# Performance work log

Measured on AMD Instinct MI355X. Metric: run time of the kernel, lower is better.

Reference implementation:

```python
import jax, jax.numpy as jnp
import numpy as np

WS = 7           # window_size
DIM_HEAD = 32    # qk head dim
NUM_HEAD = 8     # dim_in // dim_head = 256 // 32
DIM_EXP = 1024   # dim_in * exp_ratio
WIN_NUM = 16     # (28 // 7) ** 2
EPS = 1e-5


def _rel_pos_index():
    # same construction as torch buffer; returns [49*49] int index into (2*WS-1)^2 table
    coords = np.stack(np.meshgrid(np.arange(WS), np.arange(WS), indexing='ij'))  # [2,WS,WS]
    cf = coords.reshape(2, -1)                                                   # [2,49]
    rel = cf[:, :, None] - cf[:, None, :]                                        # [2,49,49]
    rel = rel.transpose(1, 2, 0)
    rel[:, :, 0] += WS - 1
    rel[:, :, 1] += WS - 1
    rel[:, :, 0] *= 2 * WS - 1
    return jnp.asarray(rel.sum(-1).reshape(-1), dtype=jnp.int32)                 # [2401]


def _ln_channel(x, w, b):
    # LayerNorm over channel dim (axis=1) of [b,c,h,w], per the 'ln_1d' norm
    mu = jnp.mean(x, axis=1, keepdims=True)
    var = jnp.var(x, axis=1, keepdims=True)
    xn = (x - mu) * jax.lax.rsqrt(var + EPS)
    return xn * w[None, :, None, None] + b[None, :, None, None]


def setup_inputs() -> dict:
    key = jax.random.key(0)
    ks = jax.random.split(key, 12)
    C = 256
    x = jax.random.normal(ks[0], (64, C, 28, 28), dtype=jnp.float32)
    return {
        'x': x,
        'pre_w': jnp.ones((C,), jnp.float32),
        'pre_b': jnp.zeros((C,), jnp.float32),
        'qk_w': jax.random.normal(ks[1], (2 * C, C), jnp.float32) * 0.02,
        'qk_b': jnp.zeros((2 * C,), jnp.float32),
        'v_w': jax.random.normal(ks[2], (DIM_EXP, C), jnp.float32) * 0.02,
        'v_b': jnp.zeros((DIM_EXP,), jnp.float32),
        'post_w': jnp.ones((DIM_EXP // 2,), jnp.float32),
        'post_b': jnp.zeros((DIM_EXP // 2,), jnp.float32),
        'proj_w': jax.random.normal(ks[3], (C, DIM_EXP), jnp.float32) * 0.02,
        'proj_b': jnp.zeros((C,), jnp.float32),
        'rpb_table': jax.random.normal(ks[4], (WIN_NUM, (2 * WS - 1) ** 2, NUM_HEAD), jnp.float32) * 0.02,
    }


def reference(x, pre_w, pre_b, qk_w, qk_b, v_w, v_b, post_w, post_b, proj_w, proj_b, rpb_table):
    B, C, H, W = x.shape
    n1, n2 = H // WS, W // WS
    shortcut = x
    # b c (h1 n1) (w1 n2) -> (b n1 n2) c h1 w1
    xw = x.reshape(B, C, WS, n1, WS, n2).transpose(0, 3, 5, 1, 2, 4).reshape(B * n1 * n2, C, WS, WS)
    b = B * n1 * n2
    xw = _ln_channel(xw, pre_w, pre_b)
    # 1x1 conv QK -> split into q,k per head: channels ordered (qk, heads, dim_head)
    qk = jnp.einsum('oc,bchw->bohw', qk_w, xw) + qk_b[None, :, None, None]
    qk = qk.reshape(b, 2, NUM_HEAD, DIM_HEAD, WS * WS).transpose(1, 0, 2, 4, 3)  # [2,b,h,49,dh]
    q, k = qk[0], qk[1]
    # 1x1 conv V -> attn half + idle half
    v = jnp.einsum('oc,bchw->bohw', v_w, xw) + v_b[None, :, None, None]
    v_attn, v_idle = jnp.split(v, 2, axis=1)                                     # each [b,512,7,7]
    dhv = (DIM_EXP // 2) // NUM_HEAD
    va = v_attn.reshape(b, NUM_HEAD, dhv, WS * WS).transpose(0, 1, 3, 2)         # [b,h,49,dhv]
    # relative position bias (gathered fresh each forward, one table per window)
    idx = _rel_pos_index()
    bias = rpb_table[:, idx, :]                                                  # [wn,2401,nh]
    bias = bias.reshape(WIN_NUM, WS * WS, WS * WS, NUM_HEAD).transpose(0, 3, 1, 2)
    bias = jnp.broadcast_to(bias[None], (B, WIN_NUM, NUM_HEAD, WS * WS, WS * WS)).reshape(b, NUM_HEAD, WS * WS, WS * WS)
    # SDPA (scale = 1/sqrt(q head dim), additive float mask)
    scale = DIM_HEAD ** -0.5
    logits = jnp.einsum('bhqd,bhkd->bhqk', q, k) * scale + bias
    attn = jax.nn.softmax(logits, axis=-1)
    out = jnp.einsum('bhqk,bhkd->bhqd', attn, va)                                # [b,h,49,dhv]
    out = out.transpose(0, 1, 3, 2).reshape(b, DIM_EXP // 2, WS, WS)
    out = _ln_channel(out, post_w, post_b)
    xc = jnp.concatenate([out, v_idle], axis=1)                                  # [b,dim_exp,7,7]
    # (b n1 n2) c h1 w1 -> b c (h1 n1) (w1 n2)
    xc = xc.reshape(B, n1, n2, DIM_EXP, WS, WS).transpose(0, 3, 4, 1, 5, 2).reshape(B, DIM_EXP, H, W)
    xc = jax.nn.gelu(xc, approximate=False)
    xc = jnp.einsum('oc,bchw->bohw', proj_w, xc) + proj_b[None, :, None, None]
    y = shortcut + xc
    return jnp.roll(y, shift=(2, 2), axis=(2, 3))
```

## Files before the change

kernel.cpp:

```cpp
#include <hip/hip_runtime.h>
#include <hip/hip_bf16.h>

typedef __bf16          bf16x8 __attribute__((ext_vector_type(8)));
typedef float           f32x4  __attribute__((ext_vector_type(4)));
typedef unsigned int    u32x2  __attribute__((ext_vector_type(2)));
typedef unsigned int    u32x4v __attribute__((ext_vector_type(4)));

#define QKW_OFF  0
#define VW_OFF   262144
#define PJW_OFF  786432
#define BIAS_OFF 1310720
#define TEMP_OFF 3407872
#define XT_OFF   70516736

#define MFMA(a,b,c) __builtin_amdgcn_mfma_f32_16x16x32_bf16((a),(b),(c),0,0,0)
#define ZERO4 ((f32x4){0.f,0.f,0.f,0.f})
#define CBAR() asm volatile("" ::: "memory")

#define SXN_AT(row, byte)      ((((row)*512 + (byte))) ^ ((((row)&7))<<4))
#define RGB(j)                 (25088 + (j)*6400)
#define RG_AT(base, row, byte) (((base) + (row)*128 + (byte)) ^ (((row)&7)<<4))
#define SC_AT(row, byte)       ((25088 + (row)*512 + (byte)) ^ (((row)&7)<<4))
#define TP_AT(row, byte)       ((((row)*256 + (byte))) ^ (((row)&15)<<4))

static __device__ __forceinline__ unsigned cvtpk(float lo, float hi){
  unsigned r;
  asm("v_cvt_pk_bf16_f32 %0, %1, %2" : "=v"(r) : "v"(lo), "v"(hi));
  return r;
}
static __device__ __forceinline__ unsigned short f2bu(float f) {
  unsigned u = __builtin_bit_cast(unsigned, f);
  return (unsigned short)((u + 0x7FFFu + ((u >> 16) & 1u)) >> 16);
}
static __device__ __forceinline__ float gelu_f(float v){
  return v / (1.f + __expf(-1.5957691216057308f*v*(1.f + 0.044715f*v*v)));
}

__global__ void emo_prep_w(const float* __restrict__ qk_w, const float* __restrict__ v_w,
                           const float* __restrict__ proj_w, unsigned short* __restrict__ w16) {
  int i = blockIdx.x * 256 + threadIdx.x;
  if (i >= 655360) return;
  float v;
  if (i < 131072)      v = qk_w[i];
  else if (i < 393216) v = v_w[i - 131072];
  else                 v = proj_w[i - 393216];
  unsigned u = __builtin_bit_cast(unsigned, v);
  w16[i] = (unsigned short)((u + 0x7FFFu + ((u >> 16) & 1u)) >> 16);
}

__global__ void emo_prep_bias(const float* __restrict__ rpb, float* __restrict__ bx) {
  const int wh = blockIdx.x;
  const int win = wh >> 3, h = wh & 7;
  for (int e = threadIdx.x; e < 4096; e += 256) {
    const int chunk = e >> 8, lane = (e >> 2) & 63, r = e & 3;
    const int mt = chunk >> 2, nt = chunk & 3;
    const int m = mt*16 + (lane >> 4)*4 + r;
    const int n = nt*16 + (lane & 15);
    float v;
    if (n >= 49)      v = -1e30f;
    else if (m >= 49) v = 0.f;
    else {
      const int dI = m/7 - n/7 + 6;
      const int dJ = m%7 - n%7 + 6;
      v = rpb[(win*169 + dI*13 + dJ)*8 + h];
    }
    bx[wh*4096 + e] = v;
  }
}

__global__ __launch_bounds__(256)
void emo_prep_x(const float* __restrict__ x, const float* __restrict__ pre_w,
                const float* __restrict__ pre_b, unsigned short* __restrict__ xt) {
  __shared__ float lv[32*257];
  __shared__ float ps1[8][32];
  __shared__ float ps2[8][32];
  const int tid = threadIdx.x, lane = tid & 63, wv = tid >> 6;
  const int l32 = lane & 31, hp = lane >> 5;
  const int chunk = blockIdx.x, b = blockIdx.y;
  const int s = chunk*32 + l32;
  const bool ok = s < 784;
  const float* xb = x + (size_t)b*200704;
  float s1 = 0.f, s2 = 0.f;
  const int c0 = wv*64 + hp*32;
  for (int ci = 0; ci < 32; ++ci) {
    const int c = c0 + ci;
    const float v = ok ? xb[c*784 + s] : 0.f;
    lv[l32*257 + c] = v;
    s1 += v; s2 += v*v;
  }
  ps1[wv*2 + hp][l32] = s1;
  ps2[wv*2 + hp][l32] = s2;
  __syncthreads();
  const int px = tid & 31, j = tid >> 5;
  const int sp = chunk*32 + px;
  if (sp < 784) {
    float t1 = 0.f, t2 = 0.f;
    #pragma unroll
    for (int k = 0; k < 8; ++k) { t1 += ps1[k][px]; t2 += ps2[k][px]; }
    const float mu = t1*(1.f/256.f);
    const float rs = rsqrtf(t2*(1.f/256.f) - mu*mu + 1e-5f);
    const int h = sp/28, w = sp - h*28;
    const int win = (h & 3)*4 + (w & 3);
    const int wpx = (h >> 2)*7 + (w >> 2);
    unsigned short* row = xt + (((size_t)b*16 + win)*49 + wpx)*256 + j*32;
    #pragma unroll
    for (int g = 0; g < 4; ++g) {
      float gg[8];
      #pragma unroll
      for (int i2 = 0; i2 < 8; ++i2) {
        const int c = j*32 + g*8 + i2;
        gg[i2] = (lv[px*257 + c] - mu)*rs*pre_w[c] + pre_b[c];
      }
      u32x4v pk = { cvtpk(gg[0],gg[1]), cvtpk(gg[2],gg[3]), cvtpk(gg[4],gg[5]), cvtpk(gg[6],gg[7]) };
      *(u32x4v*)(row + g*8) = pk;
    }
  }
}

__global__ __launch_bounds__(512, 4)
void emo_main(const float* __restrict__ qk_b,  const float* __restrict__ v_b,
              const float* __restrict__ post_w,const float* __restrict__ post_b,
              const char*  __restrict__ wsc,
              float* __restrict__ temp)
{
  extern __shared__ char smem[];
  const int tid  = threadIdx.x;
  const int lane = tid & 63;
  const int l16  = lane & 15;
  const int lk   = lane >> 4;
  const int wv   = tid >> 6;
  const int bid  = blockIdx.x;
  const int Bi   = (bid >> 3) & 63;
  const int win  = ((bid & 7) << 1) | (bid >> 9);
  const int SCR  = RGB(wv);

  {
    const unsigned short* xw = (const unsigned short*)(wsc + XT_OFF)
                             + ((size_t)Bi*16 + win)*(49*256);
    for (int p = wv; p < 49; p += 8) {
      const u32x2 d = *(const u32x2*)(xw + p*256 + lane*4);
      *(u32x2*)(smem + SXN_AT(p, lane*8)) = d;
    }
  }
  __syncthreads();

  f32x4 aq[2][4], ak[2][4];
  #pragma unroll
  for (int mt = 0; mt < 2; ++mt)
    #pragma unroll
    for (int nt = 0; nt < 4; ++nt) { aq[mt][nt] = ZERO4; ak[mt][nt] = ZERO4; }
  #pragma unroll 2
  for (int kt = 0; kt < 8; ++kt) {
    bf16x8 bx[4];
    #pragma unroll
    for (int nt = 0; nt < 4; ++nt) {
      const int row = nt*16 + l16, rc = row < 49 ? row : 48;
      bx[nt] = *(const bf16x8*)(smem + SXN_AT(rc, kt*64 + lk*16));
    }
    #pragma unroll
    for (int mt = 0; mt < 2; ++mt) {
      const bf16x8 awq = *(const bf16x8*)(wsc + QKW_OFF + (size_t)(      wv*32 + mt*16 + l16)*512 + kt*64 + lk*16);
      const bf16x8 awk = *(const bf16x8*)(wsc + QKW_OFF + (size_t)(256 + wv*32 + mt*16 + l16)*512 + kt*64 + lk*16);
      #pragma unroll
      for (int nt = 0; nt < 4; ++nt) {
        aq[mt][nt] = MFMA(awq, bx[nt], aq[mt][nt]);
        ak[mt][nt] = MFMA(awk, bx[nt], ak[mt][nt]);
      }
    }
  }
  {
    const f32x4 bq0 = *(const f32x4*)(qk_b +       wv*32 +      lk*4);
    const f32x4 bq1 = *(const f32x4*)(qk_b +       wv*32 + 16 + lk*4);
    const f32x4 bk0 = *(const f32x4*)(qk_b + 256 + wv*32 +      lk*4);
    const f32x4 bk1 = *(const f32x4*)(qk_b + 256 + wv*32 + 16 + lk*4);
    #pragma unroll
    for (int nt = 0; nt < 4; ++nt) {
      aq[0][nt] += bq0; aq[1][nt] += bq1; ak[0][nt] += bk0; ak[1][nt] += bk1;
    }
  }

  #pragma unroll
  for (int nt = 0; nt < 4; ++nt) {
    const int px = nt*16 + l16;
    if (px < 49) {
      #pragma unroll
      for (int mt = 0; mt < 2; ++mt) {
        u32x2 pq  = { cvtpk(aq[mt][nt][0], aq[mt][nt][1]), cvtpk(aq[mt][nt][2], aq[mt][nt][3]) };
        u32x2 pk2 = { cvtpk(ak[mt][nt][0], ak[mt][nt][1]), cvtpk(ak[mt][nt][2], ak[mt][nt][3]) };
        *(u32x2*)(smem + RG_AT(SCR, px,      (mt*16 + lk*4)*2)) = pq;
        *(u32x2*)(smem + RG_AT(SCR, px, 64 + (mt*16 + lk*4)*2)) = pk2;
      }
    }
  }
  CBAR();

  bf16x8 qa[4], kb[4];
  #pragma unroll
  for (int t = 0; t < 4; ++t) {
    const int row = t*16 + l16, rc = row < 49 ? row : 48;
    qa[t] = *(const bf16x8*)(smem + RG_AT(SCR, rc,      lk*16));
    kb[t] = *(const bf16x8*)(smem + RG_AT(SCR, rc, 64 + lk*16));
  }

  f32x4 s[4][4];
  {
    const float scale = 0.17677669529663689f;
    const float* bxp = (const float*)(wsc + BIAS_OFF) + (size_t)(win*8 + wv)*4096 + lane*4;
    #pragma unroll
    for (int mt = 0; mt < 4; ++mt)
      #pragma unroll
      for (int nt = 0; nt < 4; ++nt) {
        f32x4 z = MFMA(qa[mt], kb[nt], ZERO4);
        s[mt][nt] = z*scale + *(const f32x4*)(bxp + (mt*4 + nt)*256);
      }
  }
  #pragma unroll
  for (int mt = 0; mt < 4; ++mt) {
    #pragma unroll
    for (int r = 0; r < 4; ++r) {
      float mx = fmaxf(fmaxf(s[mt][0][r], s[mt][1][r]), fmaxf(s[mt][2][r], s[mt][3][r]));
      mx = fmaxf(mx, __shfl_xor(mx, 1)); mx = fmaxf(mx, __shfl_xor(mx, 2));
      mx = fmaxf(mx, __shfl_xor(mx, 4)); mx = fmaxf(mx, __shfl_xor(mx, 8));
      const float e0 = __expf(s[mt][0][r]-mx), e1 = __expf(s[mt][1][r]-mx);
      const float e2 = __expf(s[mt][2][r]-mx), e3 = __expf(s[mt][3][r]-mx);
      float sm = e0+e1+e2+e3;
      sm += __shfl_xor(sm, 1); sm += __shfl_xor(sm, 2);
      sm += __shfl_xor(sm, 4); sm += __shfl_xor(sm, 8);
      const float inv = 1.f/sm;
      s[mt][0][r] = e0*inv; s[mt][1][r] = e1*inv;
      s[mt][2][r] = e2*inv; s[mt][3][r] = e3*inv;
    }
  }
  #pragma unroll
  for (int mt = 0; mt < 4; ++mt)
    #pragma unroll
    for (int r = 0; r < 4; ++r) {
      const int q = mt*16 + lk*4 + r;
      if (q < 49) {
        #pragma unroll
        for (int nt = 0; nt < 4; ++nt)
          *(unsigned short*)(smem + RG_AT(SCR, q, (nt*16 + l16)*2)) = f2bu(s[mt][nt][r]);
      }
    }
  CBAR();

  f32x4 av[4][4];
  #pragma unroll
  for (int mt = 0; mt < 4; ++mt)
    #pragma unroll
    for (int nt = 0; nt < 4; ++nt) av[mt][nt] = ZERO4;
  #pragma unroll 2
  for (int kt = 0; kt < 8; ++kt) {
    bf16x8 ax[4], bw[4];
    #pragma unroll
    for (int t = 0; t < 4; ++t) {
      const int row = t*16 + l16, rc = row < 49 ? row : 48;
      ax[t] = *(const bf16x8*)(smem + SXN_AT(rc, kt*64 + lk*16));
      bw[t] = *(const bf16x8*)(wsc + VW_OFF + (size_t)(wv*64 + t*16 + l16)*512 + kt*64 + lk*16);
    }
    #pragma unroll
    for (int mt = 0; mt < 4; ++mt)
      #pragma unroll
      for (int nt = 0; nt < 4; ++nt) av[mt][nt] = MFMA(ax[mt], bw[nt], av[mt][nt]);
  }
  {
    #pragma unroll
    for (int nt = 0; nt < 4; ++nt) {
      const float vb = v_b[wv*64 + nt*16 + l16];
      #pragma unroll
      for (int mt = 0; mt < 4; ++mt)
        #pragma unroll
        for (int r = 0; r < 4; ++r) av[mt][nt][r] += vb;
    }
  }

  bf16x8 fpb[4][2];
  #pragma unroll
  for (int t = 0; t < 4; ++t) {
    const int row = t*16 + l16, rc = row < 49 ? row : 48;
    #pragma unroll
    for (int kt = 0; kt < 2; ++kt)
      fpb[t][kt] = *(const bf16x8*)(smem + RG_AT(SCR, rc, (kt*32 + lk*8)*2));
  }
  CBAR();

  f32x4 o[4][4];
  #pragma unroll
  for (int h2 = 0; h2 < 2; ++h2) {
    #pragma unroll
    for (int tc = 0; tc < 2; ++tc) {
      const int nt = h2*2 + tc;
      const int chrow = tc*16 + l16;
      #pragma unroll
      for (int mt = 0; mt < 4; ++mt) {
        u32x2 pv = { cvtpk(av[mt][nt][0], av[mt][nt][1]), cvtpk(av[mt][nt][2], av[mt][nt][3]) };
        *(u32x2*)(smem + RG_AT(SCR, chrow, (mt*16 + lk*4)*2)) = pv;
      }
    }
    CBAR();
    #pragma unroll
    for (int tc = 0; tc < 2; ++tc) {
      const int mtc = h2*2 + tc;
      const bf16x8 a0 = *(const bf16x8*)(smem + RG_AT(SCR, tc*16 + l16, (     lk*8)*2));
      const bf16x8 a1 = *(const bf16x8*)(smem + RG_AT(SCR, tc*16 + l16, (32 + lk*8)*2));
      #pragma unroll
      for (int nt = 0; nt < 4; ++nt) {
        f32x4 z = MFMA(a0, fpb[nt][0], ZERO4);
        o[mtc][nt] = MFMA(a1, fpb[nt][1], z);
      }
    }
    CBAR();
  }

  #pragma unroll
  for (int mtc = 0; mtc < 4; ++mtc)
    #pragma unroll
    for (int nt = 0; nt < 4; ++nt) {
      const int q = nt*16 + l16;
      if (q < 49) {
        u32x2 pk = { cvtpk(o[mtc][nt][0], o[mtc][nt][1]), cvtpk(o[mtc][nt][2], o[mtc][nt][3]) };
        *(u32x2*)(smem + RG_AT(RGB(wv), q, (mtc*16 + lk*4)*2)) = pk;
      }
    }
  __syncthreads();

  {
    const int px = tid >> 3, j = tid & 7;
    if (px < 49) {
      bf16x8 f[8];
      float s1 = 0.f, s2 = 0.f;
      #pragma unroll
      for (int c8 = 0; c8 < 8; ++c8) {
        f[c8] = *(const bf16x8*)(smem + RG_AT(RGB(j), px, c8*16));
        #pragma unroll
        for (int i = 0; i < 8; ++i) { const float v = (float)f[c8][i]; s1 += v; s2 += v*v; }
      }
      s1 += __shfl_xor(s1, 1); s1 += __shfl_xor(s1, 2); s1 += __shfl_xor(s1, 4);
      s2 += __shfl_xor(s2, 1); s2 += __shfl_xor(s2, 2); s2 += __shfl_xor(s2, 4);
      const float mu = s1*(1.f/512.f);
      const float rs = rsqrtf(s2*(1.f/512.f) - mu*mu + 1e-5f);
      #pragma unroll
      for (int c8 = 0; c8 < 8; ++c8) {
        const f32x4 pw0 = *(const f32x4*)(post_w + j*64 + c8*8);
        const f32x4 pw1 = *(const f32x4*)(post_w + j*64 + c8*8 + 4);
        const f32x4 pb0 = *(const f32x4*)(post_b + j*64 + c8*8);
        const f32x4 pb1 = *(const f32x4*)(post_b + j*64 + c8*8 + 4);
        float g[8];
        #pragma unroll
        for (int i = 0; i < 8; ++i) {
          const float v = (float)f[c8][i];
          const float w = i < 4 ? pw0[i] : pw1[i-4];
          const float b = i < 4 ? pb0[i] : pb1[i-4];
          g[i] = gelu_f((v-mu)*rs*w + b);
        }
        u32x4v pk = { cvtpk(g[0],g[1]), cvtpk(g[2],g[3]), cvtpk(g[4],g[5]), cvtpk(g[6],g[7]) };
        *(u32x4v*)(smem + RG_AT(RGB(j), px, c8*16)) = pk;
      }
    }
  }
  __syncthreads();

  f32x4 pacc[2][4];
  #pragma unroll
  for (int mt = 0; mt < 2; ++mt)
    #pragma unroll
    for (int nt = 0; nt < 4; ++nt) pacc[mt][nt] = ZERO4;
  for (int j8 = 0; j8 < 8; ++j8) {
    #pragma unroll
    for (int kt2 = 0; kt2 < 2; ++kt2) {
      bf16x8 b[4];
      #pragma unroll
      for (int nt = 0; nt < 4; ++nt) {
        const int row = nt*16 + l16, rc = row < 49 ? row : 48;
        b[nt] = *(const bf16x8*)(smem + RG_AT(RGB(j8), rc, (kt2*32 + lk*8)*2));
      }
      const int kg = j8*64 + kt2*32 + lk*8;
      #pragma unroll
      for (int mt = 0; mt < 2; ++mt) {
        const bf16x8 aw = *(const bf16x8*)(wsc + PJW_OFF + (size_t)(wv*32 + mt*16 + l16)*2048 + kg*2);
        #pragma unroll
        for (int nt = 0; nt < 4; ++nt) pacc[mt][nt] = MFMA(aw, b[nt], pacc[mt][nt]);
      }
    }
  }
  for (int half = 0; half < 2; ++half) {
    __syncthreads();
    f32x4 ia[2][4];
    #pragma unroll
    for (int mt = 0; mt < 2; ++mt)
      #pragma unroll
      for (int nt = 0; nt < 4; ++nt) ia[mt][nt] = ZERO4;
    const int r0 = 512 + half*256 + wv*32;
    #pragma unroll 2
    for (int kt = 0; kt < 8; ++kt) {
      bf16x8 b[4];
      #pragma unroll
      for (int nt = 0; nt < 4; ++nt) {
        const int row = nt*16 + l16, rc = row < 49 ? row : 48;
        b[nt] = *(const bf16x8*)(smem + SXN_AT(rc, kt*64 + lk*16));
      }
      #pragma unroll
      for (int mt = 0; mt < 2; ++mt) {
        const bf16x8 aw = *(const bf16x8*)(wsc + VW_OFF + (size_t)(r0 + mt*16 + l16)*512 + kt*64 + lk*16);
        #pragma unroll
        for (int nt = 0; nt < 4; ++nt) ia[mt][nt] = MFMA(aw, b[nt], ia[mt][nt]);
      }
    }
    #pragma unroll
    for (int mt = 0; mt < 2; ++mt) {
      const f32x4 vb = *(const f32x4*)(v_b + r0 + mt*16 + lk*4);
      #pragma unroll
      for (int nt = 0; nt < 4; ++nt) {
        const int px = nt*16 + l16;
        const int chl = wv*32 + mt*16 + lk*4;
        u32x2 pk = { cvtpk(gelu_f(ia[mt][nt][0]+vb[0]), gelu_f(ia[mt][nt][1]+vb[1])),
                     cvtpk(gelu_f(ia[mt][nt][2]+vb[2]), gelu_f(ia[mt][nt][3]+vb[3])) };
        *(u32x2*)(smem + SC_AT(px, chl*2)) = pk;
      }
    }
    __syncthreads();
    #pragma unroll 2
    for (int kt = 0; kt < 8; ++kt) {
      bf16x8 b[4];
      #pragma unroll
      for (int nt = 0; nt < 4; ++nt) {
        const int row = nt*16 + l16;
        b[nt] = *(const bf16x8*)(smem + SC_AT(row, (kt*32 + lk*8)*2));
      }
      const int kg = 512 + half*256 + kt*32 + lk*8;
      #pragma unroll
      for (int mt = 0; mt < 2; ++mt) {
        const bf16x8 aw = *(const bf16x8*)(wsc + PJW_OFF + (size_t)(wv*32 + mt*16 + l16)*2048 + kg*2);
        #pragma unroll
        for (int nt = 0; nt < 4; ++nt) pacc[mt][nt] = MFMA(aw, b[nt], pacc[mt][nt]);
      }
    }
  }

  __syncthreads();
  {
    #pragma unroll
    for (int mt = 0; mt < 2; ++mt)
      #pragma unroll
      for (int r = 0; r < 4; ++r) {
        const int row = wv*32 + mt*16 + lk*4 + r;
        #pragma unroll
        for (int nt = 0; nt < 4; ++nt)
          *(float*)(smem + TP_AT(row, (nt*16 + l16)*4)) = pacc[mt][nt][r];
      }
    CBAR();
    float* tb = temp + ((size_t)Bi*16 + win)*(256*64);
    #pragma unroll
    for (int rep = 0; rep < 8; ++rep) {
      const int idx = rep*64 + lane;
      const int row = wv*32 + (idx >> 4);
      const int ch  = idx & 15;
      *(f32x4*)(tb + row*64 + ch*4) = *(const f32x4*)(smem + TP_AT(row, ch*16));
    }
  }
}

__global__ __launch_bounds__(512)
void emo_epi(const float* __restrict__ x, const float* __restrict__ temp,
             const float* __restrict__ proj_b, float* __restrict__ out) {
  extern __shared__ float lv[];
  const int b  = blockIdx.x >> 4;
  const int ct = blockIdx.x & 15;
  const int tid = threadIdx.x, lane = tid & 63, wv = tid >> 6;
  const float* tbb = temp + (size_t)b*262144;
  for (int rr = wv; rr < 256; rr += 8) {
    const int win = rr >> 4, cc = rr & 15;
    const float v = tbb[(size_t)(win*256 + ct*16 + cc)*64 + lane];
    if (lane < 49) {
      const int ph = lane / 7, pw = lane - ph*7;
      const int h = ph*4 + (win >> 2), w = pw*4 + (win & 3);
      lv[cc*812 + h*29 + w] = v;
    }
  }
  __syncthreads();
  const float* xb = x + (size_t)b*200704;
  float* ob       = out + (size_t)b*200704;
  for (int cc = 0; cc < 16; ++cc) {
    const int c = ct*16 + cc;
    const float pb = proj_b[c];
    for (int i = tid; i < 784; i += 512) {
      const int h = i / 28, w = i - h*28;
      int hs = h - 2; if (hs < 0) hs += 28;
      int ws2 = w - 2; if (ws2 < 0) ws2 += 28;
      ob[c*784 + i] = xb[c*784 + hs*28 + ws2] + lv[cc*812 + hs*29 + ws2] + pb;
    }
  }
}

extern "C" void kernel_launch(void* const* d_in, const int* in_sizes, int n_in,
                              void* d_out, int out_size, void* d_ws, size_t ws_size,
                              hipStream_t stream) {
  const float* x      = (const float*)d_in[0];
  const float* pre_w  = (const float*)d_in[1];
  const float* pre_b  = (const float*)d_in[2];
  const float* qk_w   = (const float*)d_in[3];
  const float* qk_b   = (const float*)d_in[4];
  const float* v_w    = (const float*)d_in[5];
  const float* v_b    = (const float*)d_in[6];
  const float* post_w = (const float*)d_in[7];
  const float* post_b = (const float*)d_in[8];
  const float* proj_w = (const float*)d_in[9];
  const float* proj_b = (const float*)d_in[10];
  const float* rpb    = (const float*)d_in[11];
  float* outp = (float*)d_out;
  char* wsc = (char*)d_ws;

  hipFuncSetAttribute((const void*)emo_main, hipFuncAttributeMaxDynamicSharedMemorySize, 81920);
  hipFuncSetAttribute((const void*)emo_epi,  hipFuncAttributeMaxDynamicSharedMemorySize, 53248);

  emo_prep_w<<<2560, 256, 0, stream>>>(qk_w, v_w, proj_w, (unsigned short*)wsc);
  emo_prep_bias<<<128, 256, 0, stream>>>(rpb, (float*)(wsc + BIAS_OFF));
  emo_prep_x<<<dim3(25, 64), 256, 0, stream>>>(x, pre_w, pre_b,
                                               (unsigned short*)(wsc + XT_OFF));
  emo_main<<<1024, 512, 76288, stream>>>(qk_b, v_b, post_w, post_b,
                                         (const char*)wsc, (float*)(wsc + TEMP_OFF));
  emo_epi<<<1024, 512, 51968, stream>>>(x, (const float*)(wsc + TEMP_OFF), proj_b, outp);
}
```

Before: 325.7 us.

## Fuse epilogue residual/roll into main kernel and merge weight/bias prep kernels

The main kernel now writes the projection output directly to the final rolled positions, adding the shortcut x and proj bias in registers. This removes the temp buffer round trip and the separate epilogue kernel. The two prep kernels for weights and bias are merged into one launch to cut launch overhead. The cost is scattered, poorly coalesced 4-byte global stores and x loads from the main kernel instead of the epilogue's coalesced row writes.

```diff
diff --git a/kernel.cpp b/kernel.cpp
--- a/kernel.cpp
+++ b/kernel.cpp
@@ -10,7 +10,6 @@
 #define VW_OFF   262144
 #define PJW_OFF  786432
 #define BIAS_OFF 1310720
-#define TEMP_OFF 3407872
 #define XT_OFF   70516736
 
 #define MFMA(a,b,c) __builtin_amdgcn_mfma_f32_16x16x32_bf16((a),(b),(c),0,0,0)
@@ -21,7 +20,6 @@
 #define RGB(j)                 (25088 + (j)*6400)
 #define RG_AT(base, row, byte) (((base) + (row)*128 + (byte)) ^ (((row)&7)<<4))
 #define SC_AT(row, byte)       ((25088 + (row)*512 + (byte)) ^ (((row)&7)<<4))
-#define TP_AT(row, byte)       ((((row)*256 + (byte))) ^ (((row)&15)<<4))
 
 static __device__ __forceinline__ unsigned cvtpk(float lo, float hi){
   unsigned r;
@@ -36,35 +34,37 @@
   return v / (1.f + __expf(-1.5957691216057308f*v*(1.f + 0.044715f*v*v)));
 }
 
-__global__ void emo_prep_w(const float* __restrict__ qk_w, const float* __restrict__ v_w,
-                           const float* __restrict__ proj_w, unsigned short* __restrict__ w16) {
-  int i = blockIdx.x * 256 + threadIdx.x;
-  if (i >= 655360) return;
-  float v;
-  if (i < 131072)      v = qk_w[i];
-  else if (i < 393216) v = v_w[i - 131072];
-  else                 v = proj_w[i - 393216];
-  unsigned u = __builtin_bit_cast(unsigned, v);
-  w16[i] = (unsigned short)((u + 0x7FFFu + ((u >> 16) & 1u)) >> 16);
-}
-
-__global__ void emo_prep_bias(const float* __restrict__ rpb, float* __restrict__ bx) {
-  const int wh = blockIdx.x;
-  const int win = wh >> 3, h = wh & 7;
-  for (int e = threadIdx.x; e < 4096; e += 256) {
-    const int chunk = e >> 8, lane = (e >> 2) & 63, r = e & 3;
-    const int mt = chunk >> 2, nt = chunk & 3;
-    const int m = mt*16 + (lane >> 4)*4 + r;
-    const int n = nt*16 + (lane & 15);
+__global__ void emo_prep_wb(const float* __restrict__ qk_w, const float* __restrict__ v_w,
+                            const float* __restrict__ proj_w, const float* __restrict__ rpb,
+                            unsigned short* __restrict__ w16, float* __restrict__ bx) {
+  const int blk = blockIdx.x;
+  if (blk < 2560) {
+    int i = blk * 256 + threadIdx.x;
+    if (i >= 655360) return;
     float v;
-    if (n >= 49)      v = -1e30f;
-    else if (m >= 49) v = 0.f;
-    else {
-      const int dI = m/7 - n/7 + 6;
-      const int dJ = m%7 - n%7 + 6;
-      v = rpb[(win*169 + dI*13 + dJ)*8 + h];
-    }
-    bx[wh*4096 + e] = v;
+    if (i < 131072)      v = qk_w[i];
+    else if (i < 393216) v = v_w[i - 131072];
+    else                 v = proj_w[i - 393216];
+    unsigned u = __builtin_bit_cast(unsigned, v);
+    w16[i] = (unsigned short)((u + 0x7FFFu + ((u >> 16) & 1u)) >> 16);
+  } else {
+    const int wh = blk - 2560;
+    const int win = wh >> 3, h = wh & 7;
+    for (int e = threadIdx.x; e < 4096; e += 256) {
+      const int chunk = e >> 8, lane = (e >> 2) & 63, r = e & 3;
+      const int mt = chunk >> 2, nt = chunk & 3;
+      const int m = mt*16 + (lane >> 4)*4 + r;
+      const int n = nt*16 + (lane & 15);
+      float v;
+      if (n >= 49)      v = -1e30f;
+      else if (m >= 49) v = 0.f;
+      else {
+        const int dI = m/7 - n/7 + 6;
+        const int dJ = m%7 - n%7 + 6;
+        v = rpb[(win*169 + dI*13 + dJ)*8 + h];
+      }
+      bx[wh*4096 + e] = v;
+    }
   }
 }
 
@@ -118,10 +118,12 @@
 }
 
 __global__ __launch_bounds__(512, 4)
-void emo_main(const float* __restrict__ qk_b,  const float* __restrict__ v_b,
+void emo_main(const float* __restrict__ x,
+              const float* __restrict__ qk_b,  const float* __restrict__ v_b,
               const float* __restrict__ post_w,const float* __restrict__ post_b,
+              const float* __restrict__ proj_b,
               const char*  __restrict__ wsc,
-              float* __restrict__ temp)
+              float* __restrict__ out)
 {
   extern __shared__ char smem[];
   const int tid  = threadIdx.x;
@@ -132,6 +134,8 @@
   const int bid  = blockIdx.x;
   const int Bi   = (bid >> 3) & 63;
   const int win  = ((bid & 7) << 1) | (bid >> 9);
+  const int n1   = win >> 2, n2 = win & 3;
+  const size_t xbase = (size_t)Bi * (256*784);
   const int SCR  = RGB(wv);
 
   {
@@ -437,57 +441,31 @@
     }
   }
 
-  __syncthreads();
-  {
-    #pragma unroll
-    for (int mt = 0; mt < 2; ++mt)
+  {
+    int xoff[4], roff[4];
+    #pragma unroll
+    for (int nt = 0; nt < 4; ++nt) {
+      const int px = nt*16 + l16;
+      const int pc = px < 49 ? px : 48;
+      const int gh = (pc/7)*4 + n1, gw = (pc%7)*4 + n2;
+      xoff[nt] = gh*28 + gw;
+      int rh = gh + 2; if (rh >= 28) rh -= 28;
+      int rw = gw + 2; if (rw >= 28) rw -= 28;
+      roff[nt] = rh*28 + rw;
+    }
+    #pragma unroll
+    for (int mt = 0; mt < 2; ++mt) {
       #pragma unroll
       for (int r = 0; r < 4; ++r) {
-        const int row = wv*32 + mt*16 + lk*4 + r;
-        #pragma unroll
-        for (int nt = 0; nt < 4; ++nt)
-          *(float*)(smem + TP_AT(row, (nt*16 + l16)*4)) = pacc[mt][nt][r];
-      }
-    CBAR();
-    float* tb = temp + ((size_t)Bi*16 + win)*(256*64);
-    #pragma unroll
-    for (int rep = 0; rep < 8; ++rep) {
-      const int idx = rep*64 + lane;
-      const int row = wv*32 + (idx >> 4);
-      const int ch  = idx & 15;
-      *(f32x4*)(tb + row*64 + ch*4) = *(const f32x4*)(smem + TP_AT(row, ch*16));
-    }
-  }
-}
-
-__global__ __launch_bounds__(512)
-void emo_epi(const float* __restrict__ x, const float* __restrict__ temp,
-             const float* __restrict__ proj_b, float* __restrict__ out) {
-  extern __shared__ float lv[];
-  const int b  = blockIdx.x >> 4;
-  const int ct = blockIdx.x & 15;
-  const int tid = threadIdx.x, lane = tid & 63, wv = tid >> 6;
-  const float* tbb = temp + (size_t)b*262144;
-  for (int rr = wv; rr < 256; rr += 8) {
-    const int win = rr >> 4, cc = rr & 15;
-    const float v = tbb[(size_t)(win*256 + ct*16 + cc)*64 + lane];
-    if (lane < 49) {
-      const int ph = lane / 7, pw = lane - ph*7;
-      const int h = ph*4 + (win >> 2), w = pw*4 + (win & 3);
-      lv[cc*812 + h*29 + w] = v;
-    }
-  }
-  __syncthreads();
-  const float* xb = x + (size_t)b*200704;
-  float* ob       = out + (size_t)b*200704;
-  for (int cc = 0; cc < 16; ++cc) {
-    const int c = ct*16 + cc;
-    const float pb = proj_b[c];
-    for (int i = tid; i < 784; i += 512) {
-      const int h = i / 28, w = i - h*28;
-      int hs = h - 2; if (hs < 0) hs += 28;
-      int ws2 = w - 2; if (ws2 < 0) ws2 += 28;
-      ob[c*784 + i] = xb[c*784 + hs*28 + ws2] + lv[cc*812 + hs*29 + ws2] + pb;
+        const int o2 = wv*32 + mt*16 + lk*4 + r;
+        const float pb = proj_b[o2];
+        const size_t cb = xbase + (size_t)o2*784;
+        #pragma unroll
+        for (int nt = 0; nt < 4; ++nt) {
+          if (nt*16 + l16 < 49)
+            out[cb + roff[nt]] = x[cb + xoff[nt]] + pacc[mt][nt][r] + pb;
+        }
+      }
     }
   }
 }
@@ -511,13 +489,11 @@
   char* wsc = (char*)d_ws;
 
   hipFuncSetAttribute((const void*)emo_main, hipFuncAttributeMaxDynamicSharedMemorySize, 81920);
-  hipFuncSetAttribute((const void*)emo_epi,  hipFuncAttributeMaxDynamicSharedMemorySize, 53248);
-
-  emo_prep_w<<<2560, 256, 0, stream>>>(qk_w, v_w, proj_w, (unsigned short*)wsc);
-  emo_prep_bias<<<128, 256, 0, stream>>>(rpb, (float*)(wsc + BIAS_OFF));
+
+  emo_prep_wb<<<2688, 256, 0, stream>>>(qk_w, v_w, proj_w, rpb,
+                                        (unsigned short*)wsc, (float*)(wsc + BIAS_OFF));
   emo_prep_x<<<dim3(25, 64), 256, 0, stream>>>(x, pre_w, pre_b,
                                                (unsigned short*)(wsc + XT_OFF));
-  emo_main<<<1024, 512, 76288, stream>>>(qk_b, v_b, post_w, post_b,
-                                         (const char*)wsc, (float*)(wsc + TEMP_OFF));
-  emo_epi<<<1024, 512, 51968, stream>>>(x, (const float*)(wsc + TEMP_OFF), proj_b, outp);
-}
+  emo_main<<<1024, 512, 76288, stream>>>(x, qk_b, v_b, post_w, post_b, proj_b,
+                                         (const char*)wsc, outp);
+}
```

New measurement: 344.2 us. 5.7% more time.
